# Optimization experiments

Hardware: AMD Instinct MI355X
Metric: run time of the kernel (lower is better)

## Reference

```python
import jax, jax.numpy as jnp
import numpy as np

N, IN_F, OUT_F = 10000, 512, 64
ALPHA = 0.2       # leaky relu slope
THRESHOLD = 0.01  # hub threshold
NEG_INF = -9.0e15


def setup_inputs() -> dict:
    key = jax.random.key(0)
    k_h, k_adj, k_hub, k_W, k_as, k_ad = jax.random.split(key, 6)
    h = jax.random.normal(k_h, (N, IN_F), dtype=jnp.float32)
    adj = jax.random.randint(k_adj, (N, N), 0, 2, dtype=jnp.int32)
    hub_mask = jax.random.uniform(k_hub, (N,), dtype=jnp.float32)
    # xavier-uniform-ish params (gain 1.414)
    lim_W = 1.414 * np.sqrt(6.0 / (IN_F + OUT_F))
    W = jax.random.uniform(k_W, (IN_F, OUT_F), minval=-lim_W, maxval=lim_W, dtype=jnp.float32)
    lim_a = 1.414 * np.sqrt(6.0 / (OUT_F + 1))
    a_src = jax.random.uniform(k_as, (OUT_F, 1), minval=-lim_a, maxval=lim_a, dtype=jnp.float32)
    a_dst = jax.random.uniform(k_ad, (OUT_F, 1), minval=-lim_a, maxval=lim_a, dtype=jnp.float32)
    return {"h": h, "W": W, "a_src": a_src, "a_dst": a_dst, "hub_mask": hub_mask, "adj": adj}


def reference(h, W, a_src, a_dst, hub_mask, adj):
    Wh = h @ W                                  # [N, F_out]
    e_src = Wh @ a_src                          # [N, 1]
    e_dst = Wh @ a_dst                          # [N, 1]
    e = jax.nn.leaky_relu(e_src + e_dst.T, negative_slope=ALPHA)  # [N, N]
    scores = jnp.where(adj > 0, e, jnp.float32(NEG_INF))
    attention = jax.nn.softmax(scores, axis=1)  # row-wise softmax over neighbors
    attention = jax.nn.relu(attention - hub_mask * THRESHOLD)  # hub threshold prune
    # dropout omitted (inference mode / p applied as no-op for deterministic reference)
    h_prime = attention @ Wh                    # [N, F_out]
    return jax.nn.elu(h_prime)                  # concat=True branch
```

## Files before the change

### kernel.cpp

```cpp
#include <hip/hip_runtime.h>
#include <math.h>

#define N_NODES 10000
#define IN_FEAT 512
#define OUT_FEAT 64
#define LRELU_ALPHA 0.2f
#define HUB_THRESH 0.01f
#define BITS_WORDS 320

#define WH_OFF   0
#define ESRC_OFF 640000
#define EDST_OFF 650000
#define T_OFF    660000
#define LT_OFF   670000

__global__ __launch_bounds__(256) void k1_gemm(
    const float* __restrict__ h, const float* __restrict__ W,
    const float* __restrict__ a_src, const float* __restrict__ a_dst,
    const float* __restrict__ hub, float* __restrict__ ws)
{
    const int bx = blockIdx.x, tid = threadIdx.x;
    if (bx >= 625) {
        const int base = (bx - 625) * 1024;
        #pragma unroll
        for (int e = 0; e < 4; ++e) {
            int idx = base + e * 256 + tid;
            if (idx < N_NODES) {
                float t = hub[idx] * HUB_THRESH;
                ws[T_OFF + idx]  = t;
                ws[LT_OFF + idx] = logf(t);
            }
        }
        return;
    }

    __shared__ __align__(16) float Ws[64 * 64];
    __shared__ __align__(16) float Hs[16 * 64];
    const int col = tid & 63, rg = tid >> 6;
    const int rowBase = bx * 16;
    float acc[4] = {0.f, 0.f, 0.f, 0.f};

    for (int k0 = 0; k0 < IN_FEAT; k0 += 64) {
        for (int idx = tid; idx < 4096; idx += 256) {
            int kk = idx >> 6, c = idx & 63;
            Ws[idx] = W[(size_t)(k0 + kk) * 64 + c];
        }
        for (int idx = tid; idx < 1024; idx += 256) {
            int r = idx >> 6, kk = idx & 63;
            Hs[idx] = h[(size_t)(rowBase + r) * IN_FEAT + k0 + kk];
        }
        __syncthreads();
        #pragma unroll
        for (int k4 = 0; k4 < 16; ++k4) {
            float4 hv0 = *(const float4*)&Hs[(rg + 0)  * 64 + k4 * 4];
            float4 hv1 = *(const float4*)&Hs[(rg + 4)  * 64 + k4 * 4];
            float4 hv2 = *(const float4*)&Hs[(rg + 8)  * 64 + k4 * 4];
            float4 hv3 = *(const float4*)&Hs[(rg + 12) * 64 + k4 * 4];
            float w0 = Ws[(k4 * 4 + 0) * 64 + col];
            float w1 = Ws[(k4 * 4 + 1) * 64 + col];
            float w2 = Ws[(k4 * 4 + 2) * 64 + col];
            float w3 = Ws[(k4 * 4 + 3) * 64 + col];
            acc[0] += hv0.x * w0 + hv0.y * w1 + hv0.z * w2 + hv0.w * w3;
            acc[1] += hv1.x * w0 + hv1.y * w1 + hv1.z * w2 + hv1.w * w3;
            acc[2] += hv2.x * w0 + hv2.y * w1 + hv2.z * w2 + hv2.w * w3;
            acc[3] += hv3.x * w0 + hv3.y * w1 + hv3.z * w2 + hv3.w * w3;
        }
        __syncthreads();
    }

    const float asv = a_src[col], adv = a_dst[col];
    #pragma unroll
    for (int r = 0; r < 4; ++r) {
        int row = rowBase + rg + 4 * r;
        ws[WH_OFF + (size_t)row * 64 + col] = acc[r];
        float s1 = acc[r] * asv, s2 = acc[r] * adv;
        #pragma unroll
        for (int m = 32; m; m >>= 1) {
            s1 += __shfl_xor(s1, m, 64);
            s2 += __shfl_xor(s2, m, 64);
        }
        if (col == 0) {
            ws[ESRC_OFF + row] = s1;
            ws[EDST_OFF + row] = s2;
        }
    }
}

__global__ __launch_bounds__(256) void k2_fused(
    const int* __restrict__ adj, const float* __restrict__ ws,
    float* __restrict__ out)
{
    const int i = blockIdx.x, tid = threadIdx.x;
    const int lane = tid & 63, w = tid >> 6;
    __shared__ unsigned bits[BITS_WORDS];
    __shared__ float partA[4];
    __shared__ float partB[256];

    const float esrc = ws[ESRC_OFF + i];
    const float* __restrict__ edst = ws + EDST_OFF;
    const int4* __restrict__ arow = (const int4*)(adj + (size_t)i * N_NODES);
    float acc = 0.f;

    #pragma unroll
    for (int it = 0; it < 10; ++it) {
        const int j0 = it * 1024 + tid * 4;
        unsigned nib = 0;
        if (j0 < N_NODES) {
            int4 a4  = arow[j0 >> 2];
            float4 e4 = *(const float4*)(edst + j0);
            float s, e;
            s = esrc + e4.x; e = fmaxf(s, LRELU_ALPHA * s);
            if (a4.x > 0) { acc += __expf(e); nib |= 1u; }
            s = esrc + e4.y; e = fmaxf(s, LRELU_ALPHA * s);
            if (a4.y > 0) { acc += __expf(e); nib |= 2u; }
            s = esrc + e4.z; e = fmaxf(s, LRELU_ALPHA * s);
            if (a4.z > 0) { acc += __expf(e); nib |= 4u; }
            s = esrc + e4.w; e = fmaxf(s, LRELU_ALPHA * s);
            if (a4.w > 0) { acc += __expf(e); nib |= 8u; }
        }
        unsigned v = nib << ((lane & 7) * 4);
        v |= (unsigned)__shfl_xor((int)v, 1, 64);
        v |= (unsigned)__shfl_xor((int)v, 2, 64);
        v |= (unsigned)__shfl_xor((int)v, 4, 64);
        if ((lane & 7) == 0) bits[j0 >> 5] = v;
    }

    #pragma unroll
    for (int m = 32; m; m >>= 1) acc += __shfl_xor(acc, m, 64);
    if (lane == 0) partA[w] = acc;
    __syncthreads();
    const float l = partA[0] + partA[1] + partA[2] + partA[3];

    const bool empty = (l == 0.0f);
    const float cl = empty ? 0.0f : logf(l);
    const float invN = 1.0f / (float)N_NODES;
    const float* __restrict__ tarr  = ws + T_OFF;
    const float* __restrict__ ltarr = ws + LT_OFF;
    const float* __restrict__ Wh    = ws + WH_OFF;
    acc = 0.f;

    const int ngroups = (N_NODES + 63) >> 6;
    for (int g = w; g < ngroups; g += 4) {
        const int j = g * 64 + lane;
        const int jc = j < N_NODES ? j : N_NODES - 1;
        const unsigned word = bits[j >> 5];
        const bool bit = (word >> (j & 31)) & 1u;
        const float ed = edst[jc];
        const float s = esrc + ed;
        const float e = fmaxf(s, LRELU_ALPHA * s);
        float wgt = 0.0f;
        if (empty) {
            if (j < N_NODES) wgt = fmaxf(invN - tarr[jc], 0.0f);
        } else {
            bool cand = (j < N_NODES) && bit && (e > cl + ltarr[jc] - 0.0625f);
            if (cand) {
                float p = __expf(e - cl);
                wgt = fmaxf(p - tarr[jc], 0.0f);
            }
        }
        unsigned long long mk = __ballot(wgt > 0.0f);
        while (mk) {
            int src = __builtin_ctzll(mk);
            mk &= mk - 1;
            float wv = __shfl(wgt, src, 64);
            int jj = g * 64 + src;
            acc += wv * Wh[(size_t)jj * 64 + lane];
        }
    }

    partB[tid] = acc;
    __syncthreads();
    if (w == 0) {
        float tot = partB[lane] + partB[64 + lane] + partB[128 + lane] + partB[192 + lane];
        out[(size_t)i * 64 + lane] = tot > 0.0f ? tot : expm1f(tot);
    }
}

extern "C" void kernel_launch(void* const* d_in, const int* in_sizes, int n_in,
                              void* d_out, int out_size, void* d_ws, size_t ws_size,
                              hipStream_t stream)
{
    const float* h     = (const float*)d_in[0];
    const float* W     = (const float*)d_in[1];
    const float* a_src = (const float*)d_in[2];
    const float* a_dst = (const float*)d_in[3];
    const float* hub   = (const float*)d_in[4];
    const int*   adj   = (const int*)d_in[5];
    float* ws  = (float*)d_ws;
    float* out = (float*)d_out;

    k1_gemm<<<635, 256, 0, stream>>>(h, W, a_src, a_dst, hub, ws);
    k2_fused<<<N_NODES, 256, 0, stream>>>(adj, ws, out);
}
```

Before: 673.7 us.

## Compact surviving attention candidates into shared-memory lists before Wh accumulation

Replaces the per-64-column ballot loop in the aggregation phase with a chunked scheme. Each 1024-column chunk first filters neighbours through the bitmask and threshold tests, then appends surviving (index, weight) pairs to a double-buffered shared list using shared atomics. All four waves then split the compacted list to accumulate rows of Wh. This removes the per-group ballot and shuffle overhead and balances work across waves, at the cost of shared atomics, a barrier per chunk, and a fixed capacity of 1024 candidates per chunk.

```diff
diff --git a/kernel.cpp b/kernel.cpp
--- a/kernel.cpp
+++ b/kernel.cpp
@@ -7,6 +7,7 @@
 #define LRELU_ALPHA 0.2f
 #define HUB_THRESH 0.01f
 #define BITS_WORDS 320
+#define CAND_CAP 1024
 
 #define WH_OFF   0
 #define ESRC_OFF 640000
@@ -95,11 +96,16 @@
     __shared__ unsigned bits[BITS_WORDS];
     __shared__ float partA[4];
     __shared__ float partB[256];
+    __shared__ int   candj[2][CAND_CAP];
+    __shared__ float candw[2][CAND_CAP];
+    __shared__ int   cnt[10];
 
     const float esrc = ws[ESRC_OFF + i];
     const float* __restrict__ edst = ws + EDST_OFF;
     const int4* __restrict__ arow = (const int4*)(adj + (size_t)i * N_NODES);
     float acc = 0.f;
+
+    if (tid < 10) cnt[tid] = 0;
 
     #pragma unroll
     for (int it = 0; it < 10; ++it) {
@@ -134,41 +140,65 @@
     const bool empty = (l == 0.0f);
     const float cl = empty ? 0.0f : logf(l);
     const float invN = 1.0f / (float)N_NODES;
+    const float thr = cl - 0.0625f;
     const float* __restrict__ tarr  = ws + T_OFF;
     const float* __restrict__ ltarr = ws + LT_OFF;
     const float* __restrict__ Wh    = ws + WH_OFF;
-    acc = 0.f;
-
-    const int ngroups = (N_NODES + 63) >> 6;
-    for (int g = w; g < ngroups; g += 4) {
-        const int j = g * 64 + lane;
-        const int jc = j < N_NODES ? j : N_NODES - 1;
-        const unsigned word = bits[j >> 5];
-        const bool bit = (word >> (j & 31)) & 1u;
-        const float ed = edst[jc];
-        const float s = esrc + ed;
-        const float e = fmaxf(s, LRELU_ALPHA * s);
-        float wgt = 0.0f;
-        if (empty) {
-            if (j < N_NODES) wgt = fmaxf(invN - tarr[jc], 0.0f);
-        } else {
-            bool cand = (j < N_NODES) && bit && (e > cl + ltarr[jc] - 0.0625f);
-            if (cand) {
-                float p = __expf(e - cl);
-                wgt = fmaxf(p - tarr[jc], 0.0f);
+    float oacc = 0.f;
+
+    for (int it = 0; it < 10; ++it) {
+        const int buf = it & 1;
+        const int j0 = it * 1024 + tid * 4;
+        if (j0 < N_NODES) {
+            if (!empty) {
+                const unsigned word = bits[j0 >> 5];
+                const unsigned nib = (word >> (j0 & 31)) & 0xFu;
+                if (nib) {
+                    float4 e4  = *(const float4*)(edst + j0);
+                    float4 lt4 = *(const float4*)(ltarr + j0);
+                    #pragma unroll
+                    for (int c = 0; c < 4; ++c) {
+                        if (nib & (1u << c)) {
+                            float ed = (c == 0) ? e4.x : (c == 1) ? e4.y : (c == 2) ? e4.z : e4.w;
+                            float lt = (c == 0) ? lt4.x : (c == 1) ? lt4.y : (c == 2) ? lt4.z : lt4.w;
+                            float s = esrc + ed;
+                            float e = fmaxf(s, LRELU_ALPHA * s);
+                            if (e > thr + lt) {
+                                float p = __expf(e - cl);
+                                float wgt = p - tarr[j0 + c];
+                                if (wgt > 0.0f) {
+                                    int k = atomicAdd(&cnt[it], 1);
+                                    candj[buf][k] = j0 + c;
+                                    candw[buf][k] = wgt;
+                                }
+                            }
+                        }
+                    }
+                }
+            } else {
+                float4 t4 = *(const float4*)(tarr + j0);
+                #pragma unroll
+                for (int c = 0; c < 4; ++c) {
+                    float tv = (c == 0) ? t4.x : (c == 1) ? t4.y : (c == 2) ? t4.z : t4.w;
+                    float wgt = invN - tv;
+                    if (wgt > 0.0f) {
+                        int k = atomicAdd(&cnt[it], 1);
+                        candj[buf][k] = j0 + c;
+                        candw[buf][k] = wgt;
+                    }
+                }
             }
         }
-        unsigned long long mk = __ballot(wgt > 0.0f);
-        while (mk) {
-            int src = __builtin_ctzll(mk);
-            mk &= mk - 1;
-            float wv = __shfl(wgt, src, 64);
-            int jj = g * 64 + src;
-            acc += wv * Wh[(size_t)jj * 64 + lane];
-        }
-    }
-
-    partB[tid] = acc;
+        __syncthreads();
+        const int M = cnt[it];
+        for (int c = w; c < M; c += 4) {
+            int   jj = candj[buf][c];
+            float wv = candw[buf][c];
+            oacc += wv * Wh[(size_t)jj * 64 + lane];
+        }
+    }
+
+    partB[tid] = oacc;
     __syncthreads();
     if (w == 0) {
         float tot = partB[lane] + partB[64 + lane] + partB[128 + lane] + partB[192 + lane];
```

Measured after the change: 655.1 us. 2.7% less time.
